# Optimization experiments

Measured on AMD Instinct MI355X. Metric: run time of the kernel, lower is better.

The kernel has to match this reference:

```python
import jax, jax.numpy as jnp
import numpy as np

B, T, D = 2048, 200, 64
H1, H2 = 80, 40
NEG_INF = -4294967295.0  # -(2**32) + 1 as in original


def setup_inputs() -> dict:
    key0 = jax.random.key(0)
    ks = jax.random.split(key0, 10)
    din_dim = 4 * D
    inp = {
        "query": jax.random.normal(ks[0], (B, D), dtype=jnp.float32),
        "key": jax.random.normal(ks[1], (B, T, D), dtype=jnp.float32),
        "mask": jax.random.randint(ks[2], (B,), 1, T + 1, dtype=jnp.int32),
        # MLP params (Dense 4D->80->40->1, use_bias=True)
        "W1": jax.random.normal(ks[3], (din_dim, H1), dtype=jnp.float32) / np.sqrt(din_dim),
        "b1": jnp.zeros((H1,), dtype=jnp.float32),
        "W2": jax.random.normal(ks[4], (H1, H2), dtype=jnp.float32) / np.sqrt(H1),
        "b2": jnp.zeros((H2,), dtype=jnp.float32),
        "W3": jax.random.normal(ks[5], (H2, 1), dtype=jnp.float32) / np.sqrt(H2),
        "b3": jnp.zeros((1,), dtype=jnp.float32),
    }
    return inp


def reference(query, key, mask, W1, b1, W2, b2, W3, b3):
    b, t, d = key.shape
    q = query[:, None, :]                      # [B,1,D]
    q_tile = jnp.broadcast_to(q, (b, t, d))    # [B,T,D]
    din_all = jnp.concatenate([q_tile, key, q_tile - key, q_tile * key], axis=-1)  # [B,T,4D]
    h = jax.nn.sigmoid(jnp.einsum("btf,fh->bth", din_all, W1) + b1)
    h = jax.nn.sigmoid(jnp.einsum("bth,hg->btg", h, W2) + b2)
    score = (jnp.einsum("btg,go->bto", h, W3) + b3)[..., 0]  # [B,T]
    key_mask = jnp.arange(t)[None, :] < mask[:, None]        # [B,T]
    score = jnp.where(key_mask, score, NEG_INF)
    score = score / jnp.asarray(d, score.dtype) ** 0.5
    attn = jax.nn.softmax(score, axis=-1)                    # [B,T]
    out = jnp.einsum("bt,btd->bd", attn, key)                # [B,D] (squeezed)
    return out
```

## Files before the change

kernel.cpp:

```cpp
#include <hip/hip_runtime.h>
#include <math.h>

#define B_  2048
#define T_  200
#define D_  64
#define H1_ 80
#define H2_ 40

#define WSTR 104
#define HSTR 104

#define WS_A    0
#define WS_C    10240
#define WS_W2T  20480
#define WS_ACT  30464

typedef __bf16 bf16x8 __attribute__((ext_vector_type(8)));
typedef float  f32x4  __attribute__((ext_vector_type(4)));

__device__ __forceinline__ float sigmoidf_(float x) {
    return __builtin_amdgcn_rcpf(1.0f + __expf(-x));
}

__global__ __launch_bounds__(256)
void prep_kernel(const float* __restrict__ W1, const float* __restrict__ W2,
                 void* __restrict__ ws)
{
    __bf16* A    = (__bf16*)((char*)ws + WS_A);
    __bf16* C    = (__bf16*)((char*)ws + WS_C);
    __bf16* W2Tp = (__bf16*)((char*)ws + WS_W2T);
    float*  acT  = (float*)((char*)ws + WS_ACT);
    const int e0 = blockIdx.x * 256 + threadIdx.x;

    for (int e = e0; e < H1_ * D_; e += 2048) {
        int h = e >> 6, f = e & 63;
        float wb = W1[(64  + f) * H1_ + h];
        float wc = W1[(128 + f) * H1_ + h];
        float wd = W1[(192 + f) * H1_ + h];
        float wa = W1[f * H1_ + h];
        A[e]   = (__bf16)(wb - wc);
        C[e]   = (__bf16)wd;
        acT[e] = wa + wc;
    }
    for (int e = e0; e < 48 * WSTR; e += 2048) {
        int g = e / WSTR, h = e - g * WSTR;
        W2Tp[e] = (g < H2_ && h < H1_) ? (__bf16)W2[h * H2_ + g] : (__bf16)0.0f;
    }
}

__global__ __launch_bounds__(256, 2)
void attn_din10(const float* __restrict__ query,
                const float* __restrict__ key,
                const int*   __restrict__ mask,
                const float* __restrict__ b1,
                const float* __restrict__ b2,
                const float* __restrict__ W3,
                const float* __restrict__ b3,
                const void*  __restrict__ ws,
                float* __restrict__ out)
{
    __shared__ __align__(16) __bf16 s_h1[4][16 * HSTR];
    __shared__ __align__(16) float  s_q[4][D_];
    __shared__ float s_base[4][H1_];
    __shared__ float s_sc16[4][16];
    __shared__ float s_part[4][D_];

    const int tid  = threadIdx.x;
    const int lane = tid & 63;
    const int w    = tid >> 6;
    const int c16  = lane & 15;
    const int g16  = lane >> 4;
    const int b    = blockIdx.x * 4 + w;

    const int   mv     = mask[b];
    const int   ntiles = (mv + 15) >> 4;
    const float b3v    = b3[0];
    const float* kb = key + (size_t)b * T_ * D_;

    const __bf16* wsA   = (const __bf16*)((const char*)ws + WS_A);
    const __bf16* wsC   = (const __bf16*)((const char*)ws + WS_C);
    const __bf16* wsW2T = (const __bf16*)((const char*)ws + WS_W2T);
    const float*  wsacT = (const float*) ((const char*)ws + WS_ACT);

    float qv = query[b * D_ + lane];
    float4 u0, u1, u2, u3;
    {
        const float* kr = kb + (size_t)c16 * D_ + g16 * 8;
        u0 = *(const float4*)(kr);
        u1 = *(const float4*)(kr + 4);
        u2 = *(const float4*)(kr + 32);
        u3 = *(const float4*)(kr + 36);
    }
    s_q[w][lane] = qv;

    bf16x8 bw[3][3];
    #pragma unroll
    for (int nt = 0; nt < 3; ++nt)
        #pragma unroll
        for (int ks = 0; ks < 3; ++ks)
            bw[nt][ks] = *(const bf16x8*)&wsW2T[(nt * 16 + c16) * WSTR + ks * 32 + g16 * 8];

    float b2c[3], w3c[3];
    #pragma unroll
    for (int nt = 0; nt < 3; ++nt) {
        int g = nt * 16 + c16;
        b2c[nt] = (g < H2_) ? b2[g] : 0.0f;
        w3c[nt] = (g < H2_) ? W3[g] : 0.0f;
    }

    {
        float a0 = b1[lane], a1 = 0.0f, a2 = 0.0f, a3 = 0.0f;
        const f32x4* row = (const f32x4*)&wsacT[lane * D_];
        #pragma unroll
        for (int f4 = 0; f4 < 16; ++f4) {
            f32x4 v  = row[f4];
            f32x4 q4 = *(const f32x4*)&s_q[w][f4 * 4];
            a0 = fmaf(q4[0], v[0], a0);
            a1 = fmaf(q4[1], v[1], a1);
            a2 = fmaf(q4[2], v[2], a2);
            a3 = fmaf(q4[3], v[3], a3);
        }
        s_base[w][lane] = (a0 + a1) + (a2 + a3);
    }
    if (lane < 16) {
        int h = 64 + lane;
        float a0 = b1[h], a1 = 0.0f, a2 = 0.0f, a3 = 0.0f;
        const f32x4* row = (const f32x4*)&wsacT[h * D_];
        #pragma unroll
        for (int f4 = 0; f4 < 16; ++f4) {
            f32x4 v  = row[f4];
            f32x4 q4 = *(const f32x4*)&s_q[w][f4 * 4];
            a0 = fmaf(q4[0], v[0], a0);
            a1 = fmaf(q4[1], v[1], a1);
            a2 = fmaf(q4[2], v[2], a2);
            a3 = fmaf(q4[3], v[3], a3);
        }
        s_base[w][h] = (a0 + a1) + (a2 + a3);
    }

    bf16x8 bv[5][2];
    #pragma unroll
    for (int nt = 0; nt < 5; ++nt)
        #pragma unroll
        for (int ks = 0; ks < 2; ++ks) {
            int off = (nt * 16 + c16) * D_ + ks * 32 + g16 * 8;
            bf16x8 a8 = *(const bf16x8*)&wsA[off];
            bf16x8 c8 = *(const bf16x8*)&wsC[off];
            f32x4 q0 = *(const f32x4*)&s_q[w][ks * 32 + g16 * 8];
            f32x4 q1 = *(const f32x4*)&s_q[w][ks * 32 + g16 * 8 + 4];
            bf16x8 v8;
            v8[0] = (__bf16)((float)a8[0] + q0[0] * (float)c8[0]);
            v8[1] = (__bf16)((float)a8[1] + q0[1] * (float)c8[1]);
            v8[2] = (__bf16)((float)a8[2] + q0[2] * (float)c8[2]);
            v8[3] = (__bf16)((float)a8[3] + q0[3] * (float)c8[3]);
            v8[4] = (__bf16)((float)a8[4] + q1[0] * (float)c8[4]);
            v8[5] = (__bf16)((float)a8[5] + q1[1] * (float)c8[5]);
            v8[6] = (__bf16)((float)a8[6] + q1[2] * (float)c8[6]);
            v8[7] = (__bf16)((float)a8[7] + q1[3] * (float)c8[7]);
            bv[nt][ks] = v8;
        }

    {
        int row = lane & 15, c0 = 80 + (lane >> 4) * 4;
        *(uint2*)&s_h1[w][row * HSTR + c0] = make_uint2(0u, 0u);
    }

    float base_c[5];
    #pragma unroll
    for (int nt = 0; nt < 5; ++nt) base_c[nt] = s_base[w][nt * 16 + c16];
    __bf16* myh = &s_h1[w][0];

    float o00,o01,o02,o03,o04,o05,o06,o07,o08,o09,o10,o11,o12,o13,o14,o15;
    o00=o01=o02=o03=o04=o05=o06=o07=o08=o09=o10=o11=o12=o13=o14=o15=0.0f;
    float m_run = -1e30f, l_run = 0.0f;

    for (int tt = 0; tt < ntiles; ++tt) {
        bf16x8 af0, af1;
        af0[0] = (__bf16)u0.x; af0[1] = (__bf16)u0.y; af0[2] = (__bf16)u0.z; af0[3] = (__bf16)u0.w;
        af0[4] = (__bf16)u1.x; af0[5] = (__bf16)u1.y; af0[6] = (__bf16)u1.z; af0[7] = (__bf16)u1.w;
        af1[0] = (__bf16)u2.x; af1[1] = (__bf16)u2.y; af1[2] = (__bf16)u2.z; af1[3] = (__bf16)u2.w;
        af1[4] = (__bf16)u3.x; af1[5] = (__bf16)u3.y; af1[6] = (__bf16)u3.z; af1[7] = (__bf16)u3.w;

        float4 n0 = u0, n1 = u1, n2 = u2, n3 = u3;
        if (tt + 1 < ntiles) {
            int tr = (tt + 1) * 16 + c16;
            const float* kr = kb + (size_t)((tr < T_) ? tr : (T_ - 1)) * D_ + g16 * 8;
            n0 = *(const float4*)(kr);
            n1 = *(const float4*)(kr + 4);
            n2 = *(const float4*)(kr + 32);
            n3 = *(const float4*)(kr + 36);
        }

        #pragma unroll
        for (int nt = 0; nt < 5; ++nt) {
            float bb = base_c[nt];
            f32x4 c = { bb, bb, bb, bb };
            c = __builtin_amdgcn_mfma_f32_16x16x32_bf16(af0, bv[nt][0], c, 0, 0, 0);
            c = __builtin_amdgcn_mfma_f32_16x16x32_bf16(af1, bv[nt][1], c, 0, 0, 0);
            #pragma unroll
            for (int r = 0; r < 4; ++r)
                myh[(g16 * 4 + r) * HSTR + nt * 16 + c16] = (__bf16)sigmoidf_(c[r]);
        }

        bf16x8 a2_0 = *(const bf16x8*)&myh[c16 * HSTR + g16 * 8];
        bf16x8 a2_1 = *(const bf16x8*)&myh[c16 * HSTR + 32 + g16 * 8];
        bf16x8 a2_2 = *(const bf16x8*)&myh[c16 * HSTR + 64 + g16 * 8];
        f32x4 acc2[3];
        #pragma unroll
        for (int nt = 0; nt < 3; ++nt) {
            float bb = b2c[nt];
            f32x4 c = { bb, bb, bb, bb };
            c = __builtin_amdgcn_mfma_f32_16x16x32_bf16(a2_0, bw[nt][0], c, 0, 0, 0);
            c = __builtin_amdgcn_mfma_f32_16x16x32_bf16(a2_1, bw[nt][1], c, 0, 0, 0);
            c = __builtin_amdgcn_mfma_f32_16x16x32_bf16(a2_2, bw[nt][2], c, 0, 0, 0);
            acc2[nt] = c;
        }

        const int tb = tt * 16;
        #pragma unroll
        for (int r = 0; r < 4; ++r) {
            float partial = sigmoidf_(acc2[0][r]) * w3c[0]
                          + sigmoidf_(acc2[1][r]) * w3c[1]
                          + sigmoidf_(acc2[2][r]) * w3c[2];
            partial += __shfl_xor(partial, 1);
            partial += __shfl_xor(partial, 2);
            partial += __shfl_xor(partial, 4);
            partial += __shfl_xor(partial, 8);
            if (c16 == 0) {
                int t = tb + g16 * 4 + r;
                s_sc16[w][g16 * 4 + r] = (t < mv) ? (partial + b3v) * 0.125f : -1e30f;
            }
        }

        float s = s_sc16[w][c16];
        float tm = s;
        tm = fmaxf(tm, __shfl_xor(tm, 1));
        tm = fmaxf(tm, __shfl_xor(tm, 2));
        tm = fmaxf(tm, __shfl_xor(tm, 4));
        tm = fmaxf(tm, __shfl_xor(tm, 8));
        float m_new = fmaxf(m_run, tm);
        float alpha = __expf(m_run - m_new);
        float p = __expf(s - m_new);
        float psum = p;
        psum += __shfl_xor(psum, 1);
        psum += __shfl_xor(psum, 2);
        psum += __shfl_xor(psum, 4);
        psum += __shfl_xor(psum, 8);
        l_run = l_run * alpha + psum;
        o00 = o00 * alpha + p * u0.x;  o01 = o01 * alpha + p * u0.y;
        o02 = o02 * alpha + p * u0.z;  o03 = o03 * alpha + p * u0.w;
        o04 = o04 * alpha + p * u1.x;  o05 = o05 * alpha + p * u1.y;
        o06 = o06 * alpha + p * u1.z;  o07 = o07 * alpha + p * u1.w;
        o08 = o08 * alpha + p * u2.x;  o09 = o09 * alpha + p * u2.y;
        o10 = o10 * alpha + p * u2.z;  o11 = o11 * alpha + p * u2.w;
        o12 = o12 * alpha + p * u3.x;  o13 = o13 * alpha + p * u3.y;
        o14 = o14 * alpha + p * u3.z;  o15 = o15 * alpha + p * u3.w;
        m_run = m_new;

        u0 = n0; u1 = n1; u2 = n2; u3 = n3;
    }

    #define ORED(X) X += __shfl_xor(X,1); X += __shfl_xor(X,2); X += __shfl_xor(X,4); X += __shfl_xor(X,8);
    ORED(o00) ORED(o01) ORED(o02) ORED(o03) ORED(o04) ORED(o05) ORED(o06) ORED(o07)
    ORED(o08) ORED(o09) ORED(o10) ORED(o11) ORED(o12) ORED(o13) ORED(o14) ORED(o15)
    #undef ORED
    float inv_total = __builtin_amdgcn_rcpf(l_run);
    if (c16 == 0) {
        float* sp = &s_part[w][0];
        sp[g16 * 8 + 0] = o00;  sp[g16 * 8 + 1] = o01;
        sp[g16 * 8 + 2] = o02;  sp[g16 * 8 + 3] = o03;
        sp[g16 * 8 + 4] = o04;  sp[g16 * 8 + 5] = o05;
        sp[g16 * 8 + 6] = o06;  sp[g16 * 8 + 7] = o07;
        sp[32 + g16 * 8 + 0] = o08;  sp[32 + g16 * 8 + 1] = o09;
        sp[32 + g16 * 8 + 2] = o10;  sp[32 + g16 * 8 + 3] = o11;
        sp[32 + g16 * 8 + 4] = o12;  sp[32 + g16 * 8 + 5] = o13;
        sp[32 + g16 * 8 + 6] = o14;  sp[32 + g16 * 8 + 7] = o15;
    }
    asm volatile("s_waitcnt lgkmcnt(0)" ::: "memory");
    out[b * D_ + lane] = s_part[w][lane] * inv_total;
}

extern "C" void kernel_launch(void* const* d_in, const int* in_sizes, int n_in,
                              void* d_out, int out_size, void* d_ws, size_t ws_size,
                              hipStream_t stream)
{
    const float* query = (const float*)d_in[0];
    const float* key   = (const float*)d_in[1];
    const int*   mask  = (const int*)  d_in[2];
    const float* W1    = (const float*)d_in[3];
    const float* b1    = (const float*)d_in[4];
    const float* W2    = (const float*)d_in[5];
    const float* b2    = (const float*)d_in[6];
    const float* W3    = (const float*)d_in[7];
    const float* b3    = (const float*)d_in[8];
    float* out = (float*)d_out;

    prep_kernel<<<8, 256, 0, stream>>>(W1, W2, d_ws);
    attn_din10<<<512, 256, 0, stream>>>(query, key, mask, b1, b2, W3, b3, d_ws, out);
}
```

Measured before the change: 49.18 us.

## Process two 16-row key tiles per iteration to raise MFMA ILP

The main loop now handles 32 key rows per iteration as two independent 16-row tiles. Their MFMA chains interleave, and the online-softmax rescale runs once per 32 rows instead of once per 16. The weighted sum now reads the bf16-rounded key values instead of the fp32 ones, which reduces output precision. Register and LDS use go up, which may pressure occupancy at 2 blocks/SM. Tail waste also grows because the mask length is now rounded up to 32 rows instead of 16.

```diff
diff --git a/kernel.cpp b/kernel.cpp
--- a/kernel.cpp
+++ b/kernel.cpp
@@ -49,7 +49,7 @@
 }
 
 __global__ __launch_bounds__(256, 2)
-void attn_din10(const float* __restrict__ query,
+void attn_din11(const float* __restrict__ query,
                 const float* __restrict__ key,
                 const int*   __restrict__ mask,
                 const float* __restrict__ b1,
@@ -59,10 +59,10 @@
                 const void*  __restrict__ ws,
                 float* __restrict__ out)
 {
-    __shared__ __align__(16) __bf16 s_h1[4][16 * HSTR];
+    __shared__ __align__(16) __bf16 s_h1[4][32 * HSTR];
     __shared__ __align__(16) float  s_q[4][D_];
     __shared__ float s_base[4][H1_];
-    __shared__ float s_sc16[4][16];
+    __shared__ float s_sc[4][32];
     __shared__ float s_part[4][D_];
 
     const int tid  = threadIdx.x;
@@ -73,7 +73,7 @@
     const int b    = blockIdx.x * 4 + w;
 
     const int   mv     = mask[b];
-    const int   ntiles = (mv + 15) >> 4;
+    const int   npairs = (mv + 31) >> 5;
     const float b3v    = b3[0];
     const float* kb = key + (size_t)b * T_ * D_;
 
@@ -83,13 +83,14 @@
     const float*  wsacT = (const float*) ((const char*)ws + WS_ACT);
 
     float qv = query[b * D_ + lane];
-    float4 u0, u1, u2, u3;
+    float4 uA0, uA1, uA2, uA3, uB0, uB1, uB2, uB3;
     {
-        const float* kr = kb + (size_t)c16 * D_ + g16 * 8;
-        u0 = *(const float4*)(kr);
-        u1 = *(const float4*)(kr + 4);
-        u2 = *(const float4*)(kr + 32);
-        u3 = *(const float4*)(kr + 36);
+        const float* krA = kb + (size_t)c16 * D_ + g16 * 8;
+        const float* krB = kb + (size_t)(16 + c16) * D_ + g16 * 8;
+        uA0 = *(const float4*)(krA);      uA1 = *(const float4*)(krA + 4);
+        uA2 = *(const float4*)(krA + 32); uA3 = *(const float4*)(krA + 36);
+        uB0 = *(const float4*)(krB);      uB1 = *(const float4*)(krB + 4);
+        uB2 = *(const float4*)(krB + 32); uB3 = *(const float4*)(krB + 36);
     }
     s_q[w][lane] = qv;
 
@@ -161,8 +162,8 @@
         }
 
     {
-        int row = lane & 15, c0 = 80 + (lane >> 4) * 4;
-        *(uint2*)&s_h1[w][row * HSTR + c0] = make_uint2(0u, 0u);
+        int row = lane & 31, c0 = 80 + (lane >> 5) * 8;
+        *(uint4*)&s_h1[w][row * HSTR + c0] = make_uint4(0u, 0u, 0u, 0u);
     }
 
     float base_c[5];
@@ -174,90 +175,115 @@
     o00=o01=o02=o03=o04=o05=o06=o07=o08=o09=o10=o11=o12=o13=o14=o15=0.0f;
     float m_run = -1e30f, l_run = 0.0f;
 
-    for (int tt = 0; tt < ntiles; ++tt) {
-        bf16x8 af0, af1;
-        af0[0] = (__bf16)u0.x; af0[1] = (__bf16)u0.y; af0[2] = (__bf16)u0.z; af0[3] = (__bf16)u0.w;
-        af0[4] = (__bf16)u1.x; af0[5] = (__bf16)u1.y; af0[6] = (__bf16)u1.z; af0[7] = (__bf16)u1.w;
-        af1[0] = (__bf16)u2.x; af1[1] = (__bf16)u2.y; af1[2] = (__bf16)u2.z; af1[3] = (__bf16)u2.w;
-        af1[4] = (__bf16)u3.x; af1[5] = (__bf16)u3.y; af1[6] = (__bf16)u3.z; af1[7] = (__bf16)u3.w;
-
-        float4 n0 = u0, n1 = u1, n2 = u2, n3 = u3;
-        if (tt + 1 < ntiles) {
-            int tr = (tt + 1) * 16 + c16;
-            const float* kr = kb + (size_t)((tr < T_) ? tr : (T_ - 1)) * D_ + g16 * 8;
-            n0 = *(const float4*)(kr);
-            n1 = *(const float4*)(kr + 4);
-            n2 = *(const float4*)(kr + 32);
-            n3 = *(const float4*)(kr + 36);
+    for (int pp = 0; pp < npairs; ++pp) {
+        bf16x8 afA0, afA1, afB0, afB1;
+        afA0[0]=(__bf16)uA0.x; afA0[1]=(__bf16)uA0.y; afA0[2]=(__bf16)uA0.z; afA0[3]=(__bf16)uA0.w;
+        afA0[4]=(__bf16)uA1.x; afA0[5]=(__bf16)uA1.y; afA0[6]=(__bf16)uA1.z; afA0[7]=(__bf16)uA1.w;
+        afA1[0]=(__bf16)uA2.x; afA1[1]=(__bf16)uA2.y; afA1[2]=(__bf16)uA2.z; afA1[3]=(__bf16)uA2.w;
+        afA1[4]=(__bf16)uA3.x; afA1[5]=(__bf16)uA3.y; afA1[6]=(__bf16)uA3.z; afA1[7]=(__bf16)uA3.w;
+        afB0[0]=(__bf16)uB0.x; afB0[1]=(__bf16)uB0.y; afB0[2]=(__bf16)uB0.z; afB0[3]=(__bf16)uB0.w;
+        afB0[4]=(__bf16)uB1.x; afB0[5]=(__bf16)uB1.y; afB0[6]=(__bf16)uB1.z; afB0[7]=(__bf16)uB1.w;
+        afB1[0]=(__bf16)uB2.x; afB1[1]=(__bf16)uB2.y; afB1[2]=(__bf16)uB2.z; afB1[3]=(__bf16)uB2.w;
+        afB1[4]=(__bf16)uB3.x; afB1[5]=(__bf16)uB3.y; afB1[6]=(__bf16)uB3.z; afB1[7]=(__bf16)uB3.w;
+
+        if (pp + 1 < npairs) {
+            int trA = (pp + 1) * 32 + c16;
+            int trB = trA + 16;
+            const float* krA = kb + (size_t)((trA < T_) ? trA : (T_ - 1)) * D_ + g16 * 8;
+            const float* krB = kb + (size_t)((trB < T_) ? trB : (T_ - 1)) * D_ + g16 * 8;
+            uA0 = *(const float4*)(krA);      uA1 = *(const float4*)(krA + 4);
+            uA2 = *(const float4*)(krA + 32); uA3 = *(const float4*)(krA + 36);
+            uB0 = *(const float4*)(krB);      uB1 = *(const float4*)(krB + 4);
+            uB2 = *(const float4*)(krB + 32); uB3 = *(const float4*)(krB + 36);
         }
 
         #pragma unroll
         for (int nt = 0; nt < 5; ++nt) {
             float bb = base_c[nt];
-            f32x4 c = { bb, bb, bb, bb };
-            c = __builtin_amdgcn_mfma_f32_16x16x32_bf16(af0, bv[nt][0], c, 0, 0, 0);
-            c = __builtin_amdgcn_mfma_f32_16x16x32_bf16(af1, bv[nt][1], c, 0, 0, 0);
+            f32x4 cA = { bb, bb, bb, bb };
+            cA = __builtin_amdgcn_mfma_f32_16x16x32_bf16(afA0, bv[nt][0], cA, 0, 0, 0);
+            cA = __builtin_amdgcn_mfma_f32_16x16x32_bf16(afA1, bv[nt][1], cA, 0, 0, 0);
+            f32x4 cB = { bb, bb, bb, bb };
+            cB = __builtin_amdgcn_mfma_f32_16x16x32_bf16(afB0, bv[nt][0], cB, 0, 0, 0);
+            cB = __builtin_amdgcn_mfma_f32_16x16x32_bf16(afB1, bv[nt][1], cB, 0, 0, 0);
             #pragma unroll
-            for (int r = 0; r < 4; ++r)
-                myh[(g16 * 4 + r) * HSTR + nt * 16 + c16] = (__bf16)sigmoidf_(c[r]);
-        }
-
-        bf16x8 a2_0 = *(const bf16x8*)&myh[c16 * HSTR + g16 * 8];
-        bf16x8 a2_1 = *(const bf16x8*)&myh[c16 * HSTR + 32 + g16 * 8];
-        bf16x8 a2_2 = *(const bf16x8*)&myh[c16 * HSTR + 64 + g16 * 8];
-        f32x4 acc2[3];
+            for (int r = 0; r < 4; ++r) {
+                myh[(g16 * 4 + r) * HSTR + nt * 16 + c16]        = (__bf16)sigmoidf_(cA[r]);
+                myh[(16 + g16 * 4 + r) * HSTR + nt * 16 + c16]   = (__bf16)sigmoidf_(cB[r]);
+            }
+        }
+
+        bf16x8 a2A0 = *(const bf16x8*)&myh[c16 * HSTR + g16 * 8];
+        bf16x8 a2A1 = *(const bf16x8*)&myh[c16 * HSTR + 32 + g16 * 8];
+        bf16x8 a2A2 = *(const bf16x8*)&myh[c16 * HSTR + 64 + g16 * 8];
+        bf16x8 a2B0 = *(const bf16x8*)&myh[(16 + c16) * HSTR + g16 * 8];
+        bf16x8 a2B1 = *(const bf16x8*)&myh[(16 + c16) * HSTR + 32 + g16 * 8];
+        bf16x8 a2B2 = *(const bf16x8*)&myh[(16 + c16) * HSTR + 64 + g16 * 8];
+        f32x4 acc2A[3], acc2B[3];
         #pragma unroll
         for (int nt = 0; nt < 3; ++nt) {
             float bb = b2c[nt];
-            f32x4 c = { bb, bb, bb, bb };
-            c = __builtin_amdgcn_mfma_f32_16x16x32_bf16(a2_0, bw[nt][0], c, 0, 0, 0);
-            c = __builtin_amdgcn_mfma_f32_16x16x32_bf16(a2_1, bw[nt][1], c, 0, 0, 0);
-            c = __builtin_amdgcn_mfma_f32_16x16x32_bf16(a2_2, bw[nt][2], c, 0, 0, 0);
-            acc2[nt] = c;
-        }
-
-        const int tb = tt * 16;
+            f32x4 cA = { bb, bb, bb, bb };
+            cA = __builtin_amdgcn_mfma_f32_16x16x32_bf16(a2A0, bw[nt][0], cA, 0, 0, 0);
+            cA = __builtin_amdgcn_mfma_f32_16x16x32_bf16(a2A1, bw[nt][1], cA, 0, 0, 0);
+            cA = __builtin_amdgcn_mfma_f32_16x16x32_bf16(a2A2, bw[nt][2], cA, 0, 0, 0);
+            acc2A[nt] = cA;
+            f32x4 cB = { bb, bb, bb, bb };
+            cB = __builtin_amdgcn_mfma_f32_16x16x32_bf16(a2B0, bw[nt][0], cB, 0, 0, 0);
+            cB = __builtin_amdgcn_mfma_f32_16x16x32_bf16(a2B1, bw[nt][1], cB, 0, 0, 0);
+            cB = __builtin_amdgcn_mfma_f32_16x16x32_bf16(a2B2, bw[nt][2], cB, 0, 0, 0);
+            acc2B[nt] = cB;
+        }
+
+        const int tb = pp * 32;
         #pragma unroll
         for (int r = 0; r < 4; ++r) {
-            float partial = sigmoidf_(acc2[0][r]) * w3c[0]
-                          + sigmoidf_(acc2[1][r]) * w3c[1]
-                          + sigmoidf_(acc2[2][r]) * w3c[2];
-            partial += __shfl_xor(partial, 1);
-            partial += __shfl_xor(partial, 2);
-            partial += __shfl_xor(partial, 4);
-            partial += __shfl_xor(partial, 8);
+            float pA = sigmoidf_(acc2A[0][r]) * w3c[0]
+                     + sigmoidf_(acc2A[1][r]) * w3c[1]
+                     + sigmoidf_(acc2A[2][r]) * w3c[2];
+            float pB = sigmoidf_(acc2B[0][r]) * w3c[0]
+                     + sigmoidf_(acc2B[1][r]) * w3c[1]
+                     + sigmoidf_(acc2B[2][r]) * w3c[2];
+            pA += __shfl_xor(pA, 1);  pB += __shfl_xor(pB, 1);
+            pA += __shfl_xor(pA, 2);  pB += __shfl_xor(pB, 2);
+            pA += __shfl_xor(pA, 4);  pB += __shfl_xor(pB, 4);
+            pA += __shfl_xor(pA, 8);  pB += __shfl_xor(pB, 8);
             if (c16 == 0) {
-                int t = tb + g16 * 4 + r;
-                s_sc16[w][g16 * 4 + r] = (t < mv) ? (partial + b3v) * 0.125f : -1e30f;
+                int tA = tb + g16 * 4 + r;
+                int tB = tA + 16;
+                s_sc[w][g16 * 4 + r]      = (tA < mv) ? (pA + b3v) * 0.125f : -1e30f;
+                s_sc[w][16 + g16 * 4 + r] = (tB < mv) ? (pB + b3v) * 0.125f : -1e30f;
             }
         }
 
-        float s = s_sc16[w][c16];
-        float tm = s;
+        float sA = s_sc[w][c16];
+        float sB = s_sc[w][16 + c16];
+        float tm = fmaxf(sA, sB);
         tm = fmaxf(tm, __shfl_xor(tm, 1));
         tm = fmaxf(tm, __shfl_xor(tm, 2));
         tm = fmaxf(tm, __shfl_xor(tm, 4));
         tm = fmaxf(tm, __shfl_xor(tm, 8));
         float m_new = fmaxf(m_run, tm);
         float alpha = __expf(m_run - m_new);
-        float p = __expf(s - m_new);
-        float psum = p;
+        float pA = __expf(sA - m_new);
+        float pB = __expf(sB - m_new);
+        float psum = pA + pB;
         psum += __shfl_xor(psum, 1);
         psum += __shfl_xor(psum, 2);
         psum += __shfl_xor(psum, 4);
         psum += __shfl_xor(psum, 8);
         l_run = l_run * alpha + psum;
-        o00 = o00 * alpha + p * u0.x;  o01 = o01 * alpha + p * u0.y;
-        o02 = o02 * alpha + p * u0.z;  o03 = o03 * alpha + p * u0.w;
-        o04 = o04 * alpha + p * u1.x;  o05 = o05 * alpha + p * u1.y;
-        o06 = o06 * alpha + p * u1.z;  o07 = o07 * alpha + p * u1.w;
-        o08 = o08 * alpha + p * u2.x;  o09 = o09 * alpha + p * u2.y;
-        o10 = o10 * alpha + p * u2.z;  o11 = o11 * alpha + p * u2.w;
-        o12 = o12 * alpha + p * u3.x;  o13 = o13 * alpha + p * u3.y;
-        o14 = o14 * alpha + p * u3.z;  o15 = o15 * alpha + p * u3.w;
+        #define OUP(O, IA, IB) O = fmaf(pB, (float)(IB), fmaf(pA, (float)(IA), O * alpha));
+        OUP(o00, afA0[0], afB0[0])  OUP(o01, afA0[1], afB0[1])
+        OUP(o02, afA0[2], afB0[2])  OUP(o03, afA0[3], afB0[3])
+        OUP(o04, afA0[4], afB0[4])  OUP(o05, afA0[5], afB0[5])
+        OUP(o06, afA0[6], afB0[6])  OUP(o07, afA0[7], afB0[7])
+        OUP(o08, afA1[0], afB1[0])  OUP(o09, afA1[1], afB1[1])
+        OUP(o10, afA1[2], afB1[2])  OUP(o11, afA1[3], afB1[3])
+        OUP(o12, afA1[4], afB1[4])  OUP(o13, afA1[5], afB1[5])
+        OUP(o14, afA1[6], afB1[6])  OUP(o15, afA1[7], afB1[7])
+        #undef OUP
         m_run = m_new;
-
-        u0 = n0; u1 = n1; u2 = n2; u3 = n3;
     }
 
     #define ORED(X) X += __shfl_xor(X,1); X += __shfl_xor(X,2); X += __shfl_xor(X,4); X += __shfl_xor(X,8);
@@ -296,5 +322,5 @@
     float* out = (float*)d_out;
 
     prep_kernel<<<8, 256, 0, stream>>>(W1, W2, d_ws);
-    attn_din10<<<512, 256, 0, stream>>>(query, key, mask, b1, b2, W3, b3, d_ws, out);
+    attn_din11<<<512, 256, 0, stream>>>(query, key, mask, b1, b2, W3, b3, d_ws, out);
 }
```

After: 46.79 us. 4.9% less time.

## Software-pipeline layer-1 MFMA one tile ahead with double-buffered LDS hidden activations

Applied to the files above, without the earlier changes.

Restructures the per-wave tile loop so the first MLP layer for the next key tile is computed and written to a second LDS buffer while the current tile's second layer and online softmax run. Key loads are prefetched two tiles ahead. The weighted sum now reuses the bf16-converted key values instead of the fp32 ones. The aim is to overlap MFMA, sigmoid and LDS latency across tiles within a wave, at the cost of more registers and LDS and slightly lower precision in the output accumulation.

```diff
diff --git a/kernel.cpp b/kernel.cpp
--- a/kernel.cpp
+++ b/kernel.cpp
@@ -9,6 +9,7 @@
 
 #define WSTR 104
 #define HSTR 104
+#define HBUF (16 * HSTR)
 
 #define WS_A    0
 #define WS_C    10240
@@ -49,7 +50,7 @@
 }
 
 __global__ __launch_bounds__(256, 2)
-void attn_din10(const float* __restrict__ query,
+void attn_din15(const float* __restrict__ query,
                 const float* __restrict__ key,
                 const int*   __restrict__ mask,
                 const float* __restrict__ b1,
@@ -59,7 +60,7 @@
                 const void*  __restrict__ ws,
                 float* __restrict__ out)
 {
-    __shared__ __align__(16) __bf16 s_h1[4][16 * HSTR];
+    __shared__ __align__(16) __bf16 s_h1[4][2][HBUF];
     __shared__ __align__(16) float  s_q[4][D_];
     __shared__ float s_base[4][H1_];
     __shared__ float s_sc16[4][16];
@@ -162,49 +163,55 @@
 
     {
         int row = lane & 15, c0 = 80 + (lane >> 4) * 4;
-        *(uint2*)&s_h1[w][row * HSTR + c0] = make_uint2(0u, 0u);
+        *(uint2*)&s_h1[w][0][row * HSTR + c0] = make_uint2(0u, 0u);
+        *(uint2*)&s_h1[w][1][row * HSTR + c0] = make_uint2(0u, 0u);
     }
 
     float base_c[5];
     #pragma unroll
     for (int nt = 0; nt < 5; ++nt) base_c[nt] = s_base[w][nt * 16 + c16];
-    __bf16* myh = &s_h1[w][0];
+    __bf16* const myh0 = &s_h1[w][0][0];
 
     float o00,o01,o02,o03,o04,o05,o06,o07,o08,o09,o10,o11,o12,o13,o14,o15;
     o00=o01=o02=o03=o04=o05=o06=o07=o08=o09=o10=o11=o12=o13=o14=o15=0.0f;
     float m_run = -1e30f, l_run = 0.0f;
 
+    #define L1_STEP(AF0, AF1, DST)                                                   \
+        _Pragma("unroll")                                                            \
+        for (int nt = 0; nt < 5; ++nt) {                                             \
+            float bb = base_c[nt];                                                   \
+            f32x4 c = { bb, bb, bb, bb };                                            \
+            c = __builtin_amdgcn_mfma_f32_16x16x32_bf16(AF0, bv[nt][0], c, 0, 0, 0); \
+            c = __builtin_amdgcn_mfma_f32_16x16x32_bf16(AF1, bv[nt][1], c, 0, 0, 0); \
+            _Pragma("unroll")                                                        \
+            for (int r = 0; r < 4; ++r)                                              \
+                (DST)[(g16 * 4 + r) * HSTR + nt * 16 + c16] = (__bf16)sigmoidf_(c[r]); \
+        }
+
+    bf16x8 afc0, afc1, afn0, afn1;
+    afc0[0]=(__bf16)u0.x; afc0[1]=(__bf16)u0.y; afc0[2]=(__bf16)u0.z; afc0[3]=(__bf16)u0.w;
+    afc0[4]=(__bf16)u1.x; afc0[5]=(__bf16)u1.y; afc0[6]=(__bf16)u1.z; afc0[7]=(__bf16)u1.w;
+    afc1[0]=(__bf16)u2.x; afc1[1]=(__bf16)u2.y; afc1[2]=(__bf16)u2.z; afc1[3]=(__bf16)u2.w;
+    afc1[4]=(__bf16)u3.x; afc1[5]=(__bf16)u3.y; afc1[6]=(__bf16)u3.z; afc1[7]=(__bf16)u3.w;
+    if (ntiles > 1) {
+        int tr = 16 + c16;
+        const float* kr = kb + (size_t)((tr < T_) ? tr : (T_ - 1)) * D_ + g16 * 8;
+        u0 = *(const float4*)(kr);
+        u1 = *(const float4*)(kr + 4);
+        u2 = *(const float4*)(kr + 32);
+        u3 = *(const float4*)(kr + 36);
+    }
+    L1_STEP(afc0, afc1, myh0)
+    int cur = 0;
+
     for (int tt = 0; tt < ntiles; ++tt) {
-        bf16x8 af0, af1;
-        af0[0] = (__bf16)u0.x; af0[1] = (__bf16)u0.y; af0[2] = (__bf16)u0.z; af0[3] = (__bf16)u0.w;
-        af0[4] = (__bf16)u1.x; af0[5] = (__bf16)u1.y; af0[6] = (__bf16)u1.z; af0[7] = (__bf16)u1.w;
-        af1[0] = (__bf16)u2.x; af1[1] = (__bf16)u2.y; af1[2] = (__bf16)u2.z; af1[3] = (__bf16)u2.w;
-        af1[4] = (__bf16)u3.x; af1[5] = (__bf16)u3.y; af1[6] = (__bf16)u3.z; af1[7] = (__bf16)u3.w;
-
-        float4 n0 = u0, n1 = u1, n2 = u2, n3 = u3;
-        if (tt + 1 < ntiles) {
-            int tr = (tt + 1) * 16 + c16;
-            const float* kr = kb + (size_t)((tr < T_) ? tr : (T_ - 1)) * D_ + g16 * 8;
-            n0 = *(const float4*)(kr);
-            n1 = *(const float4*)(kr + 4);
-            n2 = *(const float4*)(kr + 32);
-            n3 = *(const float4*)(kr + 36);
-        }
-
-        #pragma unroll
-        for (int nt = 0; nt < 5; ++nt) {
-            float bb = base_c[nt];
-            f32x4 c = { bb, bb, bb, bb };
-            c = __builtin_amdgcn_mfma_f32_16x16x32_bf16(af0, bv[nt][0], c, 0, 0, 0);
-            c = __builtin_amdgcn_mfma_f32_16x16x32_bf16(af1, bv[nt][1], c, 0, 0, 0);
-            #pragma unroll
-            for (int r = 0; r < 4; ++r)
-                myh[(g16 * 4 + r) * HSTR + nt * 16 + c16] = (__bf16)sigmoidf_(c[r]);
-        }
-
-        bf16x8 a2_0 = *(const bf16x8*)&myh[c16 * HSTR + g16 * 8];
-        bf16x8 a2_1 = *(const bf16x8*)&myh[c16 * HSTR + 32 + g16 * 8];
-        bf16x8 a2_2 = *(const bf16x8*)&myh[c16 * HSTR + 64 + g16 * 8];
+        __bf16* const hcur = myh0 + cur * HBUF;
+        __bf16* const hnxt = myh0 + (cur ^ 1) * HBUF;
+
+        bf16x8 a2_0 = *(const bf16x8*)&hcur[c16 * HSTR + g16 * 8];
+        bf16x8 a2_1 = *(const bf16x8*)&hcur[c16 * HSTR + 32 + g16 * 8];
+        bf16x8 a2_2 = *(const bf16x8*)&hcur[c16 * HSTR + 64 + g16 * 8];
+
         f32x4 acc2[3];
         #pragma unroll
         for (int nt = 0; nt < 3; ++nt) {
@@ -214,6 +221,23 @@
             c = __builtin_amdgcn_mfma_f32_16x16x32_bf16(a2_1, bw[nt][1], c, 0, 0, 0);
             c = __builtin_amdgcn_mfma_f32_16x16x32_bf16(a2_2, bw[nt][2], c, 0, 0, 0);
             acc2[nt] = c;
+        }
+
+        const bool have_next = (tt + 1 < ntiles);
+        if (have_next) {
+            afn0[0]=(__bf16)u0.x; afn0[1]=(__bf16)u0.y; afn0[2]=(__bf16)u0.z; afn0[3]=(__bf16)u0.w;
+            afn0[4]=(__bf16)u1.x; afn0[5]=(__bf16)u1.y; afn0[6]=(__bf16)u1.z; afn0[7]=(__bf16)u1.w;
+            afn1[0]=(__bf16)u2.x; afn1[1]=(__bf16)u2.y; afn1[2]=(__bf16)u2.z; afn1[3]=(__bf16)u2.w;
+            afn1[4]=(__bf16)u3.x; afn1[5]=(__bf16)u3.y; afn1[6]=(__bf16)u3.z; afn1[7]=(__bf16)u3.w;
+            if (tt + 2 < ntiles) {
+                int tr = (tt + 2) * 16 + c16;
+                const float* kr = kb + (size_t)((tr < T_) ? tr : (T_ - 1)) * D_ + g16 * 8;
+                u0 = *(const float4*)(kr);
+                u1 = *(const float4*)(kr + 4);
+                u2 = *(const float4*)(kr + 32);
+                u3 = *(const float4*)(kr + 36);
+            }
+            L1_STEP(afn0, afn1, hnxt)
         }
 
         const int tb = tt * 16;
@@ -247,18 +271,20 @@
         psum += __shfl_xor(psum, 4);
         psum += __shfl_xor(psum, 8);
         l_run = l_run * alpha + psum;
-        o00 = o00 * alpha + p * u0.x;  o01 = o01 * alpha + p * u0.y;
-        o02 = o02 * alpha + p * u0.z;  o03 = o03 * alpha + p * u0.w;
-        o04 = o04 * alpha + p * u1.x;  o05 = o05 * alpha + p * u1.y;
-        o06 = o06 * alpha + p * u1.z;  o07 = o07 * alpha + p * u1.w;
-        o08 = o08 * alpha + p * u2.x;  o09 = o09 * alpha + p * u2.y;
-        o10 = o10 * alpha + p * u2.z;  o11 = o11 * alpha + p * u2.w;
-        o12 = o12 * alpha + p * u3.x;  o13 = o13 * alpha + p * u3.y;
-        o14 = o14 * alpha + p * u3.z;  o15 = o15 * alpha + p * u3.w;
+        o00 = fmaf(p, (float)afc0[0], o00 * alpha);  o01 = fmaf(p, (float)afc0[1], o01 * alpha);
+        o02 = fmaf(p, (float)afc0[2], o02 * alpha);  o03 = fmaf(p, (float)afc0[3], o03 * alpha);
+        o04 = fmaf(p, (float)afc0[4], o04 * alpha);  o05 = fmaf(p, (float)afc0[5], o05 * alpha);
+        o06 = fmaf(p, (float)afc0[6], o06 * alpha);  o07 = fmaf(p, (float)afc0[7], o07 * alpha);
+        o08 = fmaf(p, (float)afc1[0], o08 * alpha);  o09 = fmaf(p, (float)afc1[1], o09 * alpha);
+        o10 = fmaf(p, (float)afc1[2], o10 * alpha);  o11 = fmaf(p, (float)afc1[3], o11 * alpha);
+        o12 = fmaf(p, (float)afc1[4], o12 * alpha);  o13 = fmaf(p, (float)afc1[5], o13 * alpha);
+        o14 = fmaf(p, (float)afc1[6], o14 * alpha);  o15 = fmaf(p, (float)afc1[7], o15 * alpha);
         m_run = m_new;
 
-        u0 = n0; u1 = n1; u2 = n2; u3 = n3;
-    }
+        if (have_next) { afc0 = afn0; afc1 = afn1; }
+        cur ^= 1;
+    }
+    #undef L1_STEP
 
     #define ORED(X) X += __shfl_xor(X,1); X += __shfl_xor(X,2); X += __shfl_xor(X,4); X += __shfl_xor(X,8);
     ORED(o00) ORED(o01) ORED(o02) ORED(o03) ORED(o04) ORED(o05) ORED(o06) ORED(o07)
@@ -296,5 +322,5 @@
     float* out = (float*)d_out;
 
     prep_kernel<<<8, 256, 0, stream>>>(W1, W2, d_ws);
-    attn_din10<<<512, 256, 0, stream>>>(query, key, mask, b1, b2, W3, b3, d_ws, out);
+    attn_din15<<<512, 256, 0, stream>>>(query, key, mask, b1, b2, W3, b3, d_ws, out);
 }
```

Result: slower. 53.25 us (+8.3%).

## Cut register pressure: stage W2 in LDS, reuse bf16 key copy, raise occupancy

Applied to the files above, without the earlier changes.

W2 weights move from per-thread registers into shared memory and are read from LDS inside the tile loop. The separate next-tile prefetch registers are dropped by loading straight into u0..u3, and the output accumulation now reads the bf16-converted key fragments instead. The launch bound rises from 2 to 3 blocks per CU to exploit the lower register use. The cost is extra LDS reads per tile, a block-wide barrier, and weighting output accumulation with bf16-rounded key values, which lowers precision.

```diff
diff --git a/kernel.cpp b/kernel.cpp
--- a/kernel.cpp
+++ b/kernel.cpp
@@ -48,8 +48,8 @@
     }
 }
 
-__global__ __launch_bounds__(256, 2)
-void attn_din10(const float* __restrict__ query,
+__global__ __launch_bounds__(256, 3)
+void attn_din16(const float* __restrict__ query,
                 const float* __restrict__ key,
                 const int*   __restrict__ mask,
                 const float* __restrict__ b1,
@@ -59,6 +59,7 @@
                 const void*  __restrict__ ws,
                 float* __restrict__ out)
 {
+    __shared__ __align__(16) __bf16 s_W2T[48 * WSTR];
     __shared__ __align__(16) __bf16 s_h1[4][16 * HSTR];
     __shared__ __align__(16) float  s_q[4][D_];
     __shared__ float s_base[4][H1_];
@@ -79,7 +80,7 @@
 
     const __bf16* wsA   = (const __bf16*)((const char*)ws + WS_A);
     const __bf16* wsC   = (const __bf16*)((const char*)ws + WS_C);
-    const __bf16* wsW2T = (const __bf16*)((const char*)ws + WS_W2T);
+    const uint4*  wsW2T = (const uint4*) ((const char*)ws + WS_W2T);
     const float*  wsacT = (const float*) ((const char*)ws + WS_ACT);
 
     float qv = query[b * D_ + lane];
@@ -91,14 +92,16 @@
         u2 = *(const float4*)(kr + 32);
         u3 = *(const float4*)(kr + 36);
     }
+
+    {
+        uint4* dst = (uint4*)s_W2T;
+        #pragma unroll
+        for (int i = 0; i < 3; ++i) {
+            int e = tid + 256 * i;
+            if (e < 624) dst[e] = wsW2T[e];
+        }
+    }
     s_q[w][lane] = qv;
-
-    bf16x8 bw[3][3];
-    #pragma unroll
-    for (int nt = 0; nt < 3; ++nt)
-        #pragma unroll
-        for (int ks = 0; ks < 3; ++ks)
-            bw[nt][ks] = *(const bf16x8*)&wsW2T[(nt * 16 + c16) * WSTR + ks * 32 + g16 * 8];
 
     float b2c[3], w3c[3];
     #pragma unroll
@@ -170,6 +173,8 @@
     for (int nt = 0; nt < 5; ++nt) base_c[nt] = s_base[w][nt * 16 + c16];
     __bf16* myh = &s_h1[w][0];
 
+    __syncthreads();
+
     float o00,o01,o02,o03,o04,o05,o06,o07,o08,o09,o10,o11,o12,o13,o14,o15;
     o00=o01=o02=o03=o04=o05=o06=o07=o08=o09=o10=o11=o12=o13=o14=o15=0.0f;
     float m_run = -1e30f, l_run = 0.0f;
@@ -181,14 +186,13 @@
         af1[0] = (__bf16)u2.x; af1[1] = (__bf16)u2.y; af1[2] = (__bf16)u2.z; af1[3] = (__bf16)u2.w;
         af1[4] = (__bf16)u3.x; af1[5] = (__bf16)u3.y; af1[6] = (__bf16)u3.z; af1[7] = (__bf16)u3.w;
 
-        float4 n0 = u0, n1 = u1, n2 = u2, n3 = u3;
         if (tt + 1 < ntiles) {
             int tr = (tt + 1) * 16 + c16;
             const float* kr = kb + (size_t)((tr < T_) ? tr : (T_ - 1)) * D_ + g16 * 8;
-            n0 = *(const float4*)(kr);
-            n1 = *(const float4*)(kr + 4);
-            n2 = *(const float4*)(kr + 32);
-            n3 = *(const float4*)(kr + 36);
+            u0 = *(const float4*)(kr);
+            u1 = *(const float4*)(kr + 4);
+            u2 = *(const float4*)(kr + 32);
+            u3 = *(const float4*)(kr + 36);
         }
 
         #pragma unroll
@@ -210,9 +214,12 @@
         for (int nt = 0; nt < 3; ++nt) {
             float bb = b2c[nt];
             f32x4 c = { bb, bb, bb, bb };
-            c = __builtin_amdgcn_mfma_f32_16x16x32_bf16(a2_0, bw[nt][0], c, 0, 0, 0);
-            c = __builtin_amdgcn_mfma_f32_16x16x32_bf16(a2_1, bw[nt][1], c, 0, 0, 0);
-            c = __builtin_amdgcn_mfma_f32_16x16x32_bf16(a2_2, bw[nt][2], c, 0, 0, 0);
+            bf16x8 w0 = *(const bf16x8*)&s_W2T[(nt * 16 + c16) * WSTR + g16 * 8];
+            bf16x8 w1 = *(const bf16x8*)&s_W2T[(nt * 16 + c16) * WSTR + 32 + g16 * 8];
+            bf16x8 w2 = *(const bf16x8*)&s_W2T[(nt * 16 + c16) * WSTR + 64 + g16 * 8];
+            c = __builtin_amdgcn_mfma_f32_16x16x32_bf16(a2_0, w0, c, 0, 0, 0);
+            c = __builtin_amdgcn_mfma_f32_16x16x32_bf16(a2_1, w1, c, 0, 0, 0);
+            c = __builtin_amdgcn_mfma_f32_16x16x32_bf16(a2_2, w2, c, 0, 0, 0);
             acc2[nt] = c;
         }
 
@@ -247,17 +254,15 @@
         psum += __shfl_xor(psum, 4);
         psum += __shfl_xor(psum, 8);
         l_run = l_run * alpha + psum;
-        o00 = o00 * alpha + p * u0.x;  o01 = o01 * alpha + p * u0.y;
-        o02 = o02 * alpha + p * u0.z;  o03 = o03 * alpha + p * u0.w;
-        o04 = o04 * alpha + p * u1.x;  o05 = o05 * alpha + p * u1.y;
-        o06 = o06 * alpha + p * u1.z;  o07 = o07 * alpha + p * u1.w;
-        o08 = o08 * alpha + p * u2.x;  o09 = o09 * alpha + p * u2.y;
-        o10 = o10 * alpha + p * u2.z;  o11 = o11 * alpha + p * u2.w;
-        o12 = o12 * alpha + p * u3.x;  o13 = o13 * alpha + p * u3.y;
-        o14 = o14 * alpha + p * u3.z;  o15 = o15 * alpha + p * u3.w;
+        o00 = fmaf(p, (float)af0[0], o00 * alpha);  o01 = fmaf(p, (float)af0[1], o01 * alpha);
+        o02 = fmaf(p, (float)af0[2], o02 * alpha);  o03 = fmaf(p, (float)af0[3], o03 * alpha);
+        o04 = fmaf(p, (float)af0[4], o04 * alpha);  o05 = fmaf(p, (float)af0[5], o05 * alpha);
+        o06 = fmaf(p, (float)af0[6], o06 * alpha);  o07 = fmaf(p, (float)af0[7], o07 * alpha);
+        o08 = fmaf(p, (float)af1[0], o08 * alpha);  o09 = fmaf(p, (float)af1[1], o09 * alpha);
+        o10 = fmaf(p, (float)af1[2], o10 * alpha);  o11 = fmaf(p, (float)af1[3], o11 * alpha);
+        o12 = fmaf(p, (float)af1[4], o12 * alpha);  o13 = fmaf(p, (float)af1[5], o13 * alpha);
+        o14 = fmaf(p, (float)af1[6], o14 * alpha);  o15 = fmaf(p, (float)af1[7], o15 * alpha);
         m_run = m_new;
-
-        u0 = n0; u1 = n1; u2 = n2; u3 = n3;
     }
 
     #define ORED(X) X += __shfl_xor(X,1); X += __shfl_xor(X,2); X += __shfl_xor(X,4); X += __shfl_xor(X,8);
@@ -296,5 +301,5 @@
     float* out = (float*)d_out;
 
     prep_kernel<<<8, 256, 0, stream>>>(W1, W2, d_ws);
-    attn_din10<<<512, 256, 0, stream>>>(query, key, mask, b1, b2, W3, b3, d_ws, out);
+    attn_din16<<<512, 256, 0, stream>>>(query, key, mask, b1, b2, W3, b3, d_ws, out);
 }
```

Measured after the change: 70.26 us. 42.9% more time.
